# Kernel tuning notes

Measured on AMD Instinct MI355X. Metric: run time of the kernel, lower is better.

The kernel has to match this reference:

```python
import jax, jax.numpy as jnp
import numpy as np

N_CELLS, IN_DIM, HID, OUT = 65536, 128, 256, 128
MLP_H = 128   # engine MLP hidden width is hard-coded to 128 in the source
N_MORPH = 32  # min(32, n_cells//4)


def setup_inputs() -> dict:
    key = jax.random.key(0)
    ks = jax.random.split(key, 18)
    s = 0.05
    return {
        "x": jax.random.normal(ks[0], (1, IN_DIM), jnp.float32),
        "hiddens": jax.random.normal(ks[1], (N_CELLS, HID), jnp.float32) * 0.1,
        "Wa1": jax.random.normal(ks[2], (MLP_H, IN_DIM + HID), jnp.float32) * s,
        "ba1": jax.random.normal(ks[3], (MLP_H,), jnp.float32) * s,
        "Wa2": jax.random.normal(ks[4], (OUT, MLP_H), jnp.float32) * s,
        "ba2": jax.random.normal(ks[5], (OUT,), jnp.float32) * s,
        "Wg1": jax.random.normal(ks[6], (MLP_H, IN_DIM + HID), jnp.float32) * s,
        "bg1": jax.random.normal(ks[7], (MLP_H,), jnp.float32) * s,
        "Wg2": jax.random.normal(ks[8], (OUT, MLP_H), jnp.float32) * s,
        "bg2": jax.random.normal(ks[9], (OUT,), jnp.float32) * s,
        "W_ih": jax.random.normal(ks[10], (3 * HID, OUT + 1), jnp.float32) * s,
        "W_hh": jax.random.normal(ks[11], (3 * HID, HID), jnp.float32) * s,
        "b_ih": jax.random.normal(ks[12], (3 * HID,), jnp.float32) * s,
        "b_hh": jax.random.normal(ks[13], (3 * HID,), jnp.float32) * s,
        "nat_w": jnp.eye(HID, dtype=jnp.float32),  # nn.init.eye_
        "morph_w": jax.random.normal(ks[14], (N_MORPH, HID, HID), jnp.float32) * 0.02,
        "morph_src": jax.random.randint(ks[15], (N_MORPH,), 0, N_CELLS, jnp.int32),
        "morph_tgt": jax.random.randint(ks[16], (N_MORPH,), 0, N_CELLS, jnp.int32),
        "step": 0,
    }


def _forward(x, hiddens, Wa1, ba1, Wa2, ba2, Wg1, bg1, Wg2, bg2,
             W_ih, W_hh, b_ih, b_hh, nat_w, morph_w, morph_src, morph_tgt, step):
    n = hiddens.shape[0]
    # --- BenchMind, batched over all cells (x broadcast to every cell) ---
    xb = jnp.broadcast_to(x, (n, x.shape[-1]))
    combined = jnp.concatenate([xb, hiddens], axis=-1)               # [n, in+hid]
    a = jax.nn.relu(combined @ Wa1.T + ba1) @ Wa2.T + ba2            # [n, out]
    g = jax.nn.relu(combined @ Wg1.T + bg1) @ Wg2.T + bg2            # [n, out]
    out = a - g                                                       # [n, out]
    tension = jnp.mean(out * out, axis=-1, keepdims=True)            # [n, 1]
    # mem_input is detached in torch
    mem_in = jax.lax.stop_gradient(jnp.concatenate([out, tension], axis=-1))
    # --- PyTorch GRUCell math ---
    gi = mem_in @ W_ih.T + b_ih                                      # [n, 3H]
    gh = hiddens @ W_hh.T + b_hh                                     # [n, 3H]
    i_r, i_z, i_n = jnp.split(gi, 3, axis=-1)
    h_r, h_z, h_n = jnp.split(gh, 3, axis=-1)
    r = jax.nn.sigmoid(i_r + h_r)
    z = jax.nn.sigmoid(i_z + h_z)
    nn_ = jnp.tanh(i_n + r * h_n)
    hid = jax.lax.stop_gradient((1.0 - z) * nn_ + z * hiddens)       # detached new hiddens
    if step % 3 == 0:
        hid = jax.lax.stop_gradient(hid @ nat_w.T)                   # natural transformation
    # --- limit / colimit (morphism gather-transform-aggregate) ---
    limit = jnp.einsum('mij,mj->i', morph_w, hid[morph_src]) / N_MORPH
    colimit = jnp.einsum('mji,mj->i', morph_w, hid[morph_tgt]) / N_MORPH
    diff = limit - colimit
    cat_tension = jnp.mean(diff * diff)
    hid = hid + 0.05 * jax.lax.stop_gradient(diff)[None, :]
    # --- faction sync (+ debate if step > 5) ---
    n_f = min(8, n // 2)
    fs = n // n_f
    hf = hid[: n_f * fs].reshape(n_f, fs, hid.shape[-1])
    fmean = hf.mean(axis=1, keepdims=True)                           # [n_f,1,H]
    hf = 0.85 * hf + 0.15 * fmean
    if step > 5:
        global_op = hf.mean(axis=1).mean(axis=0)                     # mean of faction means
        dc = max(1, fs // 4)
        hf = hf.at[:, :dc].set(0.85 * hf[:, :dc] + 0.15 * global_op)
    hid = jnp.concatenate([hf.reshape(n_f * fs, -1), hid[n_f * fs:]], axis=0)
    # --- tension-weighted combination (weights detached: .item() in torch) ---
    t = jax.lax.stop_gradient(tension[:, 0])                         # [n]
    w = jax.nn.softmax(t, axis=0)
    combined_out = jnp.sum(w[:, None] * out, axis=0, keepdims=True)  # [1, out]
    avg_tension = jnp.mean(tension) + 0.1 * cat_tension
    return combined_out, avg_tension, hid


def reference(x, hiddens, Wa1, ba1, Wa2, ba2, Wg1, bg1, Wg2, bg2,
              W_ih, W_hh, b_ih, b_hh, nat_w, morph_w, morph_src, morph_tgt, step):
    combined_out, avg_tension, _ = _forward(
        x, hiddens, Wa1, ba1, Wa2, ba2, Wg1, bg1, Wg2, bg2,
        W_ih, W_hh, b_ih, b_hh, nat_w, morph_w, morph_src, morph_tgt, step)
    return combined_out, avg_tension
```

## Files before the change

kernel.cpp:

```cpp
#include <hip/hip_runtime.h>
#include <math.h>

#define N_CELLS 65536

#define OFF_W1B   0
#define OFF_W2A   32768
#define OFF_XW1B  49152
#define OFF_B2D   49408
#define OFF_PT    49536
#define OFF_PE    50560
#define OFF_POUT  51584
#define OFF_MI4   182656
#define OFF_TEN   190848
#define OFF_HH4   190912
#define OFF_GI    207296
#define OFF_GH    256448
#define OFF_PLIM  305600
#define OFF_PCOL  313792
#define OFF_GMSK  322048

typedef short bf16x8 __attribute__((ext_vector_type(8)));
typedef short s16x4  __attribute__((ext_vector_type(4)));
typedef float f32x4  __attribute__((ext_vector_type(4)));

__device__ __forceinline__ unsigned short f2bf(float f) {
    unsigned u = __builtin_bit_cast(unsigned, f);
    u += 0x7FFFu + ((u >> 16) & 1u);
    return (unsigned short)(u >> 16);
}

__device__ __forceinline__ bf16x8 cvt8(float4 a, float4 b) {
    bf16x8 v;
    v[0] = (short)f2bf(a.x); v[1] = (short)f2bf(a.y);
    v[2] = (short)f2bf(a.z); v[3] = (short)f2bf(a.w);
    v[4] = (short)f2bf(b.x); v[5] = (short)f2bf(b.y);
    v[6] = (short)f2bf(b.z); v[7] = (short)f2bf(b.w);
    return v;
}

__global__ __launch_bounds__(256) void k_prep(
    const float* __restrict__ x, const float* __restrict__ hiddens,
    const float* __restrict__ Wa1, const float* __restrict__ ba1,
    const float* __restrict__ Wa2, const float* __restrict__ ba2,
    const float* __restrict__ Wg1, const float* __restrict__ bg1,
    const float* __restrict__ Wg2, const float* __restrict__ bg2,
    const int* __restrict__ msrc, const int* __restrict__ mtgt,
    float* __restrict__ ws)
{
    const int b = blockIdx.x, t = threadIdx.x;
    unsigned short* w1b = (unsigned short*)(ws + OFF_W1B);
    unsigned short* w2a = (unsigned short*)(ws + OFF_W2A);
    if (b < 256) {
        const int n = b;
        const float* row = (n < 128) ? &Wa1[n * 384] : &Wg1[(n - 128) * 384];
        const int sk = t >> 3;
        w1b[(sk * 256 + n) * 8 + (t & 7)] = f2bf(row[128 + t]);
        if (n < 128) {
            float w2 = (t < 128) ? Wa2[n * 128 + t] : -Wg2[n * 128 + (t - 128)];
            w2a[(sk * 128 + n) * 8 + (t & 7)] = f2bf(w2);
        }
    } else if (b == 256) {
        const int n = t;
        const float* wr = (n < 128) ? &Wa1[n * 384] : &Wg1[(n - 128) * 384];
        float s = (n < 128) ? ba1[n] : bg1[n - 128];
        for (int j = 0; j < 128; ++j) s = fmaf(x[j], wr[j], s);
        ws[OFF_XW1B + n] = s;
        if (n < 128) ws[OFF_B2D + n] = ba2[n] - bg2[n];
    } else if (b < 321) {
        const int g = b - 257;
        const int cell = (g < 32) ? msrc[g] : mtgt[g - 32];
        ws[OFF_HH4 + (t >> 2) * 256 + g * 4 + (t & 3)] = hiddens[(size_t)cell * 256 + t];
    } else {
        unsigned long long* gm = (unsigned long long*)(ws + OFF_GMSK);
        for (int i = t; i < 1024; i += 256) gm[i] = 0ull;
        __syncthreads();
        if (t < 64) {
            const int cell = (t < 32) ? msrc[t] : mtgt[t - 32];
            atomicOr(&gm[cell >> 6], 1ull << t);
        }
    }
}

__global__ __launch_bounds__(512, 4) void k_main(
    const float* __restrict__ hiddens,
    const int* __restrict__ msrc, const int* __restrict__ mtgt,
    float* __restrict__ ws)
{
    __shared__ __align__(16) short hB[64 * 256];
    __shared__ __align__(16) short h1B[64 * 256];
    __shared__ float part[512];
    __shared__ float e_sm[64], t_sm[64];
    __shared__ int gid_sm[64];

    const int tid = threadIdx.x;
    const int lane = tid & 63, wid = tid >> 6;
    const int l15 = lane & 15, l4 = lane >> 4;
    const int blk = blockIdx.x;
    const int cell0 = blk * 64;

    if (tid < 64) gid_sm[tid] = (tid < 32) ? msrc[tid] : mtgt[tid - 32];

    const uint4* w1g = (const uint4*)(ws + OFF_W1B);
    const uint4* w2g = (const uint4*)(ws + OFF_W2A);

    uint4 aw0 = w1g[l4 * 256 + wid * 32 + l15];
    uint4 aw1 = w1g[l4 * 256 + wid * 32 + 16 + l15];

    {
        const int c = tid >> 3;
        const float* src = hiddens + (size_t)(cell0 + c) * 256 + (tid & 7) * 32;
        float4 va[4], vb[4];
#pragma unroll
        for (int it = 0; it < 4; ++it) {
            va[it] = *(const float4*)(src + it * 8);
            vb[it] = *(const float4*)(src + it * 8 + 4);
        }
#pragma unroll
        for (int it = 0; it < 4; ++it) {
            const int chunk = (tid & 7) * 4 + it;
            *(bf16x8*)&hB[c * 256 + ((chunk ^ (c & 7)) << 3)] = cvt8(va[it], vb[it]);
        }
    }
    __syncthreads();

    f32x4 acc[2][4];
#pragma unroll
    for (int nt = 0; nt < 2; ++nt)
#pragma unroll
        for (int ct = 0; ct < 4; ++ct) acc[nt][ct] = (f32x4)0.f;

#pragma unroll
    for (int s = 0; s < 8; ++s) {
        uint4 an0, an1;
        if (s < 7) {
            an0 = w1g[((s + 1) * 4 + l4) * 256 + wid * 32 + l15];
            an1 = w1g[((s + 1) * 4 + l4) * 256 + wid * 32 + 16 + l15];
        } else {
            an0 = w2g[l4 * 128 + wid * 16 + l15];
            an1 = an0;
        }
        bf16x8 bfr[4];
#pragma unroll
        for (int ct = 0; ct < 4; ++ct) {
            const int c = ct * 16 + l15;
            bfr[ct] = *(const bf16x8*)&hB[c * 256 + (((s * 4 + l4) ^ (l15 & 7)) << 3)];
        }
        const bf16x8 af0 = __builtin_bit_cast(bf16x8, aw0);
        const bf16x8 af1 = __builtin_bit_cast(bf16x8, aw1);
#pragma unroll
        for (int ct = 0; ct < 4; ++ct) {
            acc[0][ct] = __builtin_amdgcn_mfma_f32_16x16x32_bf16(af0, bfr[ct], acc[0][ct], 0, 0, 0);
            acc[1][ct] = __builtin_amdgcn_mfma_f32_16x16x32_bf16(af1, bfr[ct], acc[1][ct], 0, 0, 0);
        }
        aw0 = an0; aw1 = an1;
    }

    {
        float4 xb[2];
        xb[0] = *(const float4*)(ws + OFF_XW1B + wid * 32 + l4 * 4);
        xb[1] = *(const float4*)(ws + OFF_XW1B + wid * 32 + 16 + l4 * 4);
#pragma unroll
        for (int nt = 0; nt < 2; ++nt) {
            const int n0 = wid * 32 + nt * 16 + l4 * 4;
            const int chunk = n0 >> 3;
            const float bx[4] = {xb[nt].x, xb[nt].y, xb[nt].z, xb[nt].w};
#pragma unroll
            for (int ct = 0; ct < 4; ++ct) {
                const int c = ct * 16 + l15;
                s16x4 pk;
#pragma unroll
                for (int r = 0; r < 4; ++r)
                    pk[r] = (short)f2bf(fmaxf(acc[nt][ct][r] + bx[r], 0.f));
                *(s16x4*)&h1B[c * 256 + ((chunk ^ (l15 & 7)) << 3) + (l4 & 1) * 4] = pk;
            }
        }
    }
    __syncthreads();

    f32x4 acc2[4];
#pragma unroll
    for (int ct = 0; ct < 4; ++ct) acc2[ct] = (f32x4)0.f;

    uint4 a2 = aw0;
#pragma unroll
    for (int s = 0; s < 8; ++s) {
        uint4 a2n;
        if (s < 7) a2n = w2g[((s + 1) * 4 + l4) * 128 + wid * 16 + l15];
        bf16x8 b2[4];
#pragma unroll
        for (int ct = 0; ct < 4; ++ct) {
            const int c = ct * 16 + l15;
            b2[ct] = *(const bf16x8*)&h1B[c * 256 + (((s * 4 + l4) ^ (l15 & 7)) << 3)];
        }
        const bf16x8 af = __builtin_bit_cast(bf16x8, a2);
#pragma unroll
        for (int ct = 0; ct < 4; ++ct)
            acc2[ct] = __builtin_amdgcn_mfma_f32_16x16x32_bf16(af, b2[ct], acc2[ct], 0, 0, 0);
        a2 = a2n;
    }

    float outv[4][4];
    {
        float4 bd = *(const float4*)(ws + OFF_B2D + wid * 16 + l4 * 4);
        const float bv[4] = {bd.x, bd.y, bd.z, bd.w};
#pragma unroll
        for (int ct = 0; ct < 4; ++ct)
#pragma unroll
            for (int r = 0; r < 4; ++r)
                outv[ct][r] = acc2[ct][r] + bv[r];
    }

#pragma unroll
    for (int ct = 0; ct < 4; ++ct) {
        float sq = 0.f;
#pragma unroll
        for (int r = 0; r < 4; ++r) sq = fmaf(outv[ct][r], outv[ct][r], sq);
        sq += __shfl_xor(sq, 16);
        sq += __shfl_xor(sq, 32);
        if (l4 == 0) part[wid * 64 + ct * 16 + l15] = sq;
    }
    __syncthreads();

    const unsigned long long* gm = (const unsigned long long*)(ws + OFF_GMSK);
    if (tid < 64) {
        float s = 0.f;
#pragma unroll
        for (int w = 0; w < 8; ++w) s += part[w * 64 + tid];
        const float tv = s * (1.f / 128.f);
        const float ev = expf(tv);
        t_sm[tid] = tv; e_sm[tid] = ev;
        float pt = tv, pe = ev;
        for (int off = 32; off > 0; off >>= 1) {
            pt += __shfl_down(pt, off);
            pe += __shfl_down(pe, off);
        }
        if (tid == 0) { ws[OFF_PT + blk] = pt; ws[OFF_PE + blk] = pe; }
        unsigned long long m = gm[blk];
        while (m) {
            const int g = __builtin_ctzll(m); m &= m - 1;
            const int cg = gid_sm[g];
            if ((cg >> 6) == blk && (cg & 63) == tid) ws[OFF_TEN + g] = tv;
        }
    }
    __syncthreads();

    {
        float p[4];
#pragma unroll
        for (int r = 0; r < 4; ++r) {
            float s = 0.f;
#pragma unroll
            for (int ct = 0; ct < 4; ++ct)
                s = fmaf(e_sm[ct * 16 + l15], outv[ct][r], s);
            p[r] = s;
        }
#pragma unroll
        for (int r = 0; r < 4; ++r) {
            p[r] += __shfl_xor(p[r], 1);
            p[r] += __shfl_xor(p[r], 2);
            p[r] += __shfl_xor(p[r], 4);
            p[r] += __shfl_xor(p[r], 8);
        }
        if (l15 == 0)
            *(float4*)(ws + OFF_POUT + blk * 128 + wid * 16 + l4 * 4) =
                make_float4(p[0], p[1], p[2], p[3]);
    }

    {
        unsigned long long m = gm[blk];
        while (m) {
            const int g = __builtin_ctzll(m); m &= m - 1;
            const int cg = gid_sm[g];
            if ((cg >> 6) != blk) continue;
            const int c = cg & 63;
            if ((c & 15) == l15) {
                const int ct = c >> 4;
                *(float4*)(ws + OFF_MI4 + (wid * 4 + l4) * 256 + g * 4) =
                    make_float4(outv[ct][0], outv[ct][1], outv[ct][2], outv[ct][3]);
            }
        }
    }
}

__global__ __launch_bounds__(256) void k_tail1(
    const float* __restrict__ W_ih, const float* __restrict__ W_hh,
    const float* __restrict__ b_ih, const float* __restrict__ b_hh,
    float* __restrict__ ws)
{
    const int lane = threadIdx.x & 63;
    const int w    = threadIdx.x >> 6;
    const int row  = __builtin_amdgcn_readfirstlane(blockIdx.x * 4 + w);
    const float* mi4 = ws + OFF_MI4;
    const float* hh4 = ws + OFF_HH4;

    const float* wi = W_ih + row * 129;
    float gi = b_ih[row];
#pragma unroll 8
    for (int q = 0; q < 32; ++q) {
        float4 a = *(const float4*)(mi4 + q * 256 + lane * 4);
        gi = fmaf(wi[4 * q + 0], a.x, gi);
        gi = fmaf(wi[4 * q + 1], a.y, gi);
        gi = fmaf(wi[4 * q + 2], a.z, gi);
        gi = fmaf(wi[4 * q + 3], a.w, gi);
    }
    gi = fmaf(ws[OFF_TEN + lane], wi[128], gi);

    const float* wh = W_hh + (size_t)row * 256;
    float gh = b_hh[row];
#pragma unroll 8
    for (int q = 0; q < 64; ++q) {
        float4 a = *(const float4*)(hh4 + q * 256 + lane * 4);
        float4 b = *(const float4*)(wh + 4 * q);
        gh = fmaf(b.x, a.x, gh);
        gh = fmaf(b.y, a.y, gh);
        gh = fmaf(b.z, a.z, gh);
        gh = fmaf(b.w, a.w, gh);
    }
    ws[OFF_GI + row * 64 + lane] = gi;
    ws[OFF_GH + row * 64 + lane] = gh;
}

__global__ __launch_bounds__(512) void k_tail2(
    const float* __restrict__ nat_w, const float* __restrict__ morph_w,
    const int* __restrict__ step, float* __restrict__ ws)
{
    __shared__ float hd[2][256];
    __shared__ float hn[2][256];
    const int tid = threadIdx.x, half = tid >> 8, t = tid & 255, m = blockIdx.x;
    const int g = half * 32 + m;

    const float i_r = ws[OFF_GI + (0 * 256 + t) * 64 + g];
    const float i_z = ws[OFF_GI + (1 * 256 + t) * 64 + g];
    const float i_n = ws[OFF_GI + (2 * 256 + t) * 64 + g];
    const float h_r = ws[OFF_GH + (0 * 256 + t) * 64 + g];
    const float h_z = ws[OFF_GH + (1 * 256 + t) * 64 + g];
    const float h_n = ws[OFF_GH + (2 * 256 + t) * 64 + g];
    const float hv  = ws[OFF_HH4 + (t >> 2) * 256 + g * 4 + (t & 3)];

    const float r  = 1.f / (1.f + expf(-(i_r + h_r)));
    const float z  = 1.f / (1.f + expf(-(i_z + h_z)));
    const float nn = tanhf(i_n + r * h_n);
    const float hid = (1.f - z) * nn + z * hv;

    hd[half][t] = hid;
    __syncthreads();
    if (step[0] % 3 == 0) {
        const float4* wr = (const float4*)(nat_w + (size_t)t * 256);
        float s = 0.f;
        for (int q = 0; q < 64; ++q) {
            float4 wq = wr[q];
            s = fmaf(wq.x, hd[half][4 * q + 0], s);
            s = fmaf(wq.y, hd[half][4 * q + 1], s);
            s = fmaf(wq.z, hd[half][4 * q + 2], s);
            s = fmaf(wq.w, hd[half][4 * q + 3], s);
        }
        hn[half][t] = s;
    } else {
        hn[half][t] = hid;
    }
    __syncthreads();

    const float* wm = morph_w + (size_t)m * 65536;
    if (half == 0) {
        const float4* r_ = (const float4*)(wm + (size_t)t * 256);
        float L = 0.f;
        for (int q = 0; q < 64; ++q) {
            float4 wq = r_[q];
            L = fmaf(wq.x, hn[0][4 * q + 0], L);
            L = fmaf(wq.y, hn[0][4 * q + 1], L);
            L = fmaf(wq.z, hn[0][4 * q + 2], L);
            L = fmaf(wq.w, hn[0][4 * q + 3], L);
        }
        ws[OFF_PLIM + m * 256 + t] = L;
    } else {
        float C = 0.f;
        for (int j = 0; j < 256; ++j)
            C = fmaf(wm[j * 256 + t], hn[1][j], C);
        ws[OFF_PCOL + m * 256 + t] = C;
    }
}

__global__ __launch_bounds__(256) void k_out(const float* __restrict__ ws,
                                             float* __restrict__ out)
{
    __shared__ float red[256];
    const int b = blockIdx.x, t = threadIdx.x;
    if (b < 128) {
        float so = 0.f, se = 0.f;
        for (int i = t; i < 1024; i += 256) {
            so += ws[OFF_POUT + i * 128 + b];
            se += ws[OFF_PE + i];
        }
        red[t] = so; __syncthreads();
        for (int s = 128; s > 0; s >>= 1) { if (t < s) red[t] += red[t + s]; __syncthreads(); }
        const float SO = red[0]; __syncthreads();
        red[t] = se; __syncthreads();
        for (int s = 128; s > 0; s >>= 1) { if (t < s) red[t] += red[t + s]; __syncthreads(); }
        if (t == 0) out[b] = SO / red[0];
    } else {
        float pt = 0.f;
        for (int i = t; i < 1024; i += 256) pt += ws[OFF_PT + i];
        float L = 0.f, C = 0.f;
        for (int m = 0; m < 32; ++m) {
            L += ws[OFF_PLIM + m * 256 + t];
            C += ws[OFF_PCOL + m * 256 + t];
        }
        const float d = (L - C) * (1.f / 32.f);
        red[t] = d * d; __syncthreads();
        for (int s = 128; s > 0; s >>= 1) { if (t < s) red[t] += red[t + s]; __syncthreads(); }
        const float cat = red[0] * (1.f / 256.f); __syncthreads();
        red[t] = pt; __syncthreads();
        for (int s = 128; s > 0; s >>= 1) { if (t < s) red[t] += red[t + s]; __syncthreads(); }
        if (t == 0) out[128] = red[0] * (1.f / 65536.f) + 0.1f * cat;
    }
}

extern "C" void kernel_launch(void* const* d_in, const int* in_sizes, int n_in,
                              void* d_out, int out_size, void* d_ws, size_t ws_size,
                              hipStream_t stream)
{
    const float* x     = (const float*)d_in[0];
    const float* hidd  = (const float*)d_in[1];
    const float* Wa1   = (const float*)d_in[2];
    const float* ba1   = (const float*)d_in[3];
    const float* Wa2   = (const float*)d_in[4];
    const float* ba2   = (const float*)d_in[5];
    const float* Wg1   = (const float*)d_in[6];
    const float* bg1   = (const float*)d_in[7];
    const float* Wg2   = (const float*)d_in[8];
    const float* bg2   = (const float*)d_in[9];
    const float* W_ih  = (const float*)d_in[10];
    const float* W_hh  = (const float*)d_in[11];
    const float* b_ih  = (const float*)d_in[12];
    const float* b_hh  = (const float*)d_in[13];
    const float* nat_w = (const float*)d_in[14];
    const float* mw    = (const float*)d_in[15];
    const int*   msrc  = (const int*)d_in[16];
    const int*   mtgt  = (const int*)d_in[17];
    const int*   step  = (const int*)d_in[18];

    float* out = (float*)d_out;
    float* ws  = (float*)d_ws;

    k_prep <<<322, 256, 0, stream>>>(x, hidd, Wa1, ba1, Wa2, ba2, Wg1, bg1, Wg2, bg2, msrc, mtgt, ws);
    k_main <<<1024, 512, 0, stream>>>(hidd, msrc, mtgt, ws);
    k_tail1<<<192, 256, 0, stream>>>(W_ih, W_hh, b_ih, b_hh, ws);
    k_tail2<<<32, 512, 0, stream>>>(nat_w, mw, step, ws);
    k_out  <<<129, 256, 0, stream>>>(ws, out);
}
```

Baseline: 82.40 us.

## Make main kernel persistent over four tiles and restructure GRU/morph tail kernels

The main MLP kernel now handles four 64-cell tiles per block. It keeps all weight fragments in registers and prefetches the next tile's hidden rows while the current tile computes, and it pads the LDS row stride. The GRU tail is rewritten as one block per gathered cell, and the morph kernel is split into 256 blocks that stage weight chunks in LDS so column access coalesces. This aims to cut per-block weight reloads and the long serial tail kernels. The cost is fewer blocks, higher register pressure, and more partial sums for k_out to reduce.

```diff
diff --git a/kernel.cpp b/kernel.cpp
--- a/kernel.cpp
+++ b/kernel.cpp
@@ -1,7 +1,5 @@
 #include <hip/hip_runtime.h>
 #include <math.h>
-
-#define N_CELLS 65536
 
 #define OFF_W1B   0
 #define OFF_W2A   32768
@@ -10,18 +8,18 @@
 #define OFF_PT    49536
 #define OFF_PE    50560
 #define OFF_POUT  51584
-#define OFF_MI4   182656
-#define OFF_TEN   190848
-#define OFF_HH4   190912
-#define OFF_GI    207296
-#define OFF_GH    256448
-#define OFF_PLIM  305600
-#define OFF_PCOL  313792
-#define OFF_GMSK  322048
+#define OFF_MIG   182656
+#define OFF_HN    191104
+#define OFF_PLIM  207488
+#define OFF_PCOL8 215680
+#define OFF_GMSK  281216
 
 typedef short bf16x8 __attribute__((ext_vector_type(8)));
 typedef short s16x4  __attribute__((ext_vector_type(4)));
 typedef float f32x4  __attribute__((ext_vector_type(4)));
+
+#define HSTR 264
+#define POS(kc, c) ((((kc)) & 24) | ((((kc)) ^ ((c))) & 7))
 
 __device__ __forceinline__ unsigned short f2bf(float f) {
     unsigned u = __builtin_bit_cast(unsigned, f);
@@ -39,7 +37,7 @@
 }
 
 __global__ __launch_bounds__(256) void k_prep(
-    const float* __restrict__ x, const float* __restrict__ hiddens,
+    const float* __restrict__ x,
     const float* __restrict__ Wa1, const float* __restrict__ ba1,
     const float* __restrict__ Wa2, const float* __restrict__ ba2,
     const float* __restrict__ Wg1, const float* __restrict__ bg1,
@@ -53,11 +51,11 @@
     if (b < 256) {
         const int n = b;
         const float* row = (n < 128) ? &Wa1[n * 384] : &Wg1[(n - 128) * 384];
-        const int sk = t >> 3;
-        w1b[(sk * 256 + n) * 8 + (t & 7)] = f2bf(row[128 + t]);
+        const int kc = t >> 3;
+        w1b[(kc * 256 + n) * 8 + (t & 7)] = f2bf(row[128 + t]);
         if (n < 128) {
             float w2 = (t < 128) ? Wa2[n * 128 + t] : -Wg2[n * 128 + (t - 128)];
-            w2a[(sk * 128 + n) * 8 + (t & 7)] = f2bf(w2);
+            w2a[(kc * 128 + n) * 8 + (t & 7)] = f2bf(w2);
         }
     } else if (b == 256) {
         const int n = t;
@@ -66,10 +64,6 @@
         for (int j = 0; j < 128; ++j) s = fmaf(x[j], wr[j], s);
         ws[OFF_XW1B + n] = s;
         if (n < 128) ws[OFF_B2D + n] = ba2[n] - bg2[n];
-    } else if (b < 321) {
-        const int g = b - 257;
-        const int cell = (g < 32) ? msrc[g] : mtgt[g - 32];
-        ws[OFF_HH4 + (t >> 2) * 256 + g * 4 + (t & 3)] = hiddens[(size_t)cell * 256 + t];
     } else {
         unsigned long long* gm = (unsigned long long*)(ws + OFF_GMSK);
         for (int i = t; i < 1024; i += 256) gm[i] = 0ull;
@@ -81,302 +75,315 @@
     }
 }
 
-__global__ __launch_bounds__(512, 4) void k_main(
+__global__ __launch_bounds__(512, 2) void k_main(
     const float* __restrict__ hiddens,
     const int* __restrict__ msrc, const int* __restrict__ mtgt,
     float* __restrict__ ws)
 {
-    __shared__ __align__(16) short hB[64 * 256];
-    __shared__ __align__(16) short h1B[64 * 256];
+    __shared__ __align__(16) short hB[64 * HSTR];
+    __shared__ __align__(16) short h1B[64 * HSTR];
     __shared__ float part[512];
-    __shared__ float e_sm[64], t_sm[64];
+    __shared__ float e_sm[64], t_sm_[64];
     __shared__ int gid_sm[64];
 
-    const int tid = threadIdx.x;
+    const int tid  = threadIdx.x;
     const int lane = tid & 63, wid = tid >> 6;
     const int l15 = lane & 15, l4 = lane >> 4;
     const int blk = blockIdx.x;
-    const int cell0 = blk * 64;
+    const int cell0 = blk * 256;
 
     if (tid < 64) gid_sm[tid] = (tid < 32) ? msrc[tid] : mtgt[tid - 32];
 
     const uint4* w1g = (const uint4*)(ws + OFF_W1B);
     const uint4* w2g = (const uint4*)(ws + OFF_W2A);
 
-    uint4 aw0 = w1g[l4 * 256 + wid * 32 + l15];
-    uint4 aw1 = w1g[l4 * 256 + wid * 32 + 16 + l15];
-
-    {
-        const int c = tid >> 3;
-        const float* src = hiddens + (size_t)(cell0 + c) * 256 + (tid & 7) * 32;
-        float4 va[4], vb[4];
-#pragma unroll
-        for (int it = 0; it < 4; ++it) {
-            va[it] = *(const float4*)(src + it * 8);
-            vb[it] = *(const float4*)(src + it * 8 + 4);
-        }
-#pragma unroll
-        for (int it = 0; it < 4; ++it) {
-            const int chunk = (tid & 7) * 4 + it;
-            *(bf16x8*)&hB[c * 256 + ((chunk ^ (c & 7)) << 3)] = cvt8(va[it], vb[it]);
-        }
-    }
+    uint4 aw[8][2], a2[8];
+#pragma unroll
+    for (int s = 0; s < 8; ++s) {
+        aw[s][0] = w1g[(s * 4 + l4) * 256 + wid * 32 + l15];
+        aw[s][1] = w1g[(s * 4 + l4) * 256 + wid * 32 + 16 + l15];
+        a2[s]    = w2g[(s * 4 + l4) * 128 + wid * 16 + l15];
+    }
+
+    const int rc = tid >> 3;
+    const int cb = (tid & 7) * 32;
+    const float* hsrc = hiddens + (size_t)(cell0 + rc) * 256 + cb;
+
+    float4 nx[8];
+#pragma unroll
+    for (int it = 0; it < 8; ++it) nx[it] = *(const float4*)(hsrc + it * 4);
+#pragma unroll
+    for (int it = 0; it < 4; ++it) {
+        const int kc = (tid & 7) * 4 + it;
+        *(bf16x8*)&hB[rc * HSTR + POS(kc, rc) * 8] = cvt8(nx[2 * it], nx[2 * it + 1]);
+    }
+#pragma unroll
+    for (int it = 0; it < 8; ++it)
+        nx[it] = *(const float4*)(hsrc + 64 * 256 + it * 4);
     __syncthreads();
 
-    f32x4 acc[2][4];
-#pragma unroll
-    for (int nt = 0; nt < 2; ++nt)
-#pragma unroll
-        for (int ct = 0; ct < 4; ++ct) acc[nt][ct] = (f32x4)0.f;
-
-#pragma unroll
-    for (int s = 0; s < 8; ++s) {
-        uint4 an0, an1;
-        if (s < 7) {
-            an0 = w1g[((s + 1) * 4 + l4) * 256 + wid * 32 + l15];
-            an1 = w1g[((s + 1) * 4 + l4) * 256 + wid * 32 + 16 + l15];
-        } else {
-            an0 = w2g[l4 * 128 + wid * 16 + l15];
-            an1 = an0;
-        }
-        bf16x8 bfr[4];
-#pragma unroll
-        for (int ct = 0; ct < 4; ++ct) {
-            const int c = ct * 16 + l15;
-            bfr[ct] = *(const bf16x8*)&hB[c * 256 + (((s * 4 + l4) ^ (l15 & 7)) << 3)];
-        }
-        const bf16x8 af0 = __builtin_bit_cast(bf16x8, aw0);
-        const bf16x8 af1 = __builtin_bit_cast(bf16x8, aw1);
-#pragma unroll
-        for (int ct = 0; ct < 4; ++ct) {
-            acc[0][ct] = __builtin_amdgcn_mfma_f32_16x16x32_bf16(af0, bfr[ct], acc[0][ct], 0, 0, 0);
-            acc[1][ct] = __builtin_amdgcn_mfma_f32_16x16x32_bf16(af1, bfr[ct], acc[1][ct], 0, 0, 0);
-        }
-        aw0 = an0; aw1 = an1;
-    }
-
-    {
-        float4 xb[2];
-        xb[0] = *(const float4*)(ws + OFF_XW1B + wid * 32 + l4 * 4);
-        xb[1] = *(const float4*)(ws + OFF_XW1B + wid * 32 + 16 + l4 * 4);
-#pragma unroll
-        for (int nt = 0; nt < 2; ++nt) {
-            const int n0 = wid * 32 + nt * 16 + l4 * 4;
-            const int chunk = n0 >> 3;
-            const float bx[4] = {xb[nt].x, xb[nt].y, xb[nt].z, xb[nt].w};
+    float4 xb0 = *(const float4*)(ws + OFF_XW1B + wid * 32 + l4 * 4);
+    float4 xb1 = *(const float4*)(ws + OFF_XW1B + wid * 32 + 16 + l4 * 4);
+    float4 bd  = *(const float4*)(ws + OFF_B2D + wid * 16 + l4 * 4);
+    const float bdv[4] = {bd.x, bd.y, bd.z, bd.w};
+    const unsigned long long* gm = (const unsigned long long*)(ws + OFF_GMSK);
+
+    for (int t = 0; t < 4; ++t) {
+        const int bt = blk * 4 + t;
+
+        f32x4 acc[2][4];
+#pragma unroll
+        for (int nt = 0; nt < 2; ++nt)
+#pragma unroll
+            for (int ct = 0; ct < 4; ++ct) acc[nt][ct] = (f32x4)0.f;
+#pragma unroll
+        for (int s = 0; s < 8; ++s) {
+            bf16x8 bfr[4];
 #pragma unroll
             for (int ct = 0; ct < 4; ++ct) {
                 const int c = ct * 16 + l15;
-                s16x4 pk;
-#pragma unroll
-                for (int r = 0; r < 4; ++r)
-                    pk[r] = (short)f2bf(fmaxf(acc[nt][ct][r] + bx[r], 0.f));
-                *(s16x4*)&h1B[c * 256 + ((chunk ^ (l15 & 7)) << 3) + (l4 & 1) * 4] = pk;
-            }
-        }
-    }
-    __syncthreads();
-
-    f32x4 acc2[4];
-#pragma unroll
-    for (int ct = 0; ct < 4; ++ct) acc2[ct] = (f32x4)0.f;
-
-    uint4 a2 = aw0;
-#pragma unroll
-    for (int s = 0; s < 8; ++s) {
-        uint4 a2n;
-        if (s < 7) a2n = w2g[((s + 1) * 4 + l4) * 128 + wid * 16 + l15];
-        bf16x8 b2[4];
+                bfr[ct] = *(const bf16x8*)&hB[c * HSTR + POS(s * 4 + l4, c) * 8];
+            }
+            const bf16x8 af0 = __builtin_bit_cast(bf16x8, aw[s][0]);
+            const bf16x8 af1 = __builtin_bit_cast(bf16x8, aw[s][1]);
+#pragma unroll
+            for (int ct = 0; ct < 4; ++ct) {
+                acc[0][ct] = __builtin_amdgcn_mfma_f32_16x16x32_bf16(af0, bfr[ct], acc[0][ct], 0, 0, 0);
+                acc[1][ct] = __builtin_amdgcn_mfma_f32_16x16x32_bf16(af1, bfr[ct], acc[1][ct], 0, 0, 0);
+            }
+        }
+
+        {
+            const float b0[4] = {xb0.x, xb0.y, xb0.z, xb0.w};
+            const float b1[4] = {xb1.x, xb1.y, xb1.z, xb1.w};
+#pragma unroll
+            for (int nt = 0; nt < 2; ++nt) {
+                const int ch2 = wid * 4 + nt * 2 + (l4 >> 1);
+                const float* bb = nt ? b1 : b0;
+#pragma unroll
+                for (int ct = 0; ct < 4; ++ct) {
+                    const int c = ct * 16 + l15;
+                    s16x4 pk;
+#pragma unroll
+                    for (int r = 0; r < 4; ++r)
+                        pk[r] = (short)f2bf(fmaxf(acc[nt][ct][r] + bb[r], 0.f));
+                    *(s16x4*)&h1B[c * HSTR + POS(ch2, c) * 8 + (l4 & 1) * 4] = pk;
+                }
+            }
+        }
+        __syncthreads();
+
+        f32x4 acc2[4];
+#pragma unroll
+        for (int ct = 0; ct < 4; ++ct) acc2[ct] = (f32x4)0.f;
+#pragma unroll
+        for (int s = 0; s < 8; ++s) {
+            bf16x8 b2[4];
+#pragma unroll
+            for (int ct = 0; ct < 4; ++ct) {
+                const int c = ct * 16 + l15;
+                b2[ct] = *(const bf16x8*)&h1B[c * HSTR + POS(s * 4 + l4, c) * 8];
+            }
+            const bf16x8 af = __builtin_bit_cast(bf16x8, a2[s]);
+#pragma unroll
+            for (int ct = 0; ct < 4; ++ct)
+                acc2[ct] = __builtin_amdgcn_mfma_f32_16x16x32_bf16(af, b2[ct], acc2[ct], 0, 0, 0);
+        }
+
+        if (t < 3) {
+#pragma unroll
+            for (int it = 0; it < 4; ++it) {
+                const int kc = (tid & 7) * 4 + it;
+                *(bf16x8*)&hB[rc * HSTR + POS(kc, rc) * 8] = cvt8(nx[2 * it], nx[2 * it + 1]);
+            }
+            if (t < 2) {
+#pragma unroll
+                for (int it = 0; it < 8; ++it)
+                    nx[it] = *(const float4*)(hsrc + (size_t)(t + 2) * 64 * 256 + it * 4);
+            }
+        }
+
+        float outv[4][4];
+#pragma unroll
+        for (int ct = 0; ct < 4; ++ct)
+#pragma unroll
+            for (int r = 0; r < 4; ++r)
+                outv[ct][r] = acc2[ct][r] + bdv[r];
+
 #pragma unroll
         for (int ct = 0; ct < 4; ++ct) {
-            const int c = ct * 16 + l15;
-            b2[ct] = *(const bf16x8*)&h1B[c * 256 + (((s * 4 + l4) ^ (l15 & 7)) << 3)];
-        }
-        const bf16x8 af = __builtin_bit_cast(bf16x8, a2);
-#pragma unroll
-        for (int ct = 0; ct < 4; ++ct)
-            acc2[ct] = __builtin_amdgcn_mfma_f32_16x16x32_bf16(af, b2[ct], acc2[ct], 0, 0, 0);
-        a2 = a2n;
-    }
-
-    float outv[4][4];
-    {
-        float4 bd = *(const float4*)(ws + OFF_B2D + wid * 16 + l4 * 4);
-        const float bv[4] = {bd.x, bd.y, bd.z, bd.w};
-#pragma unroll
-        for (int ct = 0; ct < 4; ++ct)
-#pragma unroll
-            for (int r = 0; r < 4; ++r)
-                outv[ct][r] = acc2[ct][r] + bv[r];
-    }
-
-#pragma unroll
-    for (int ct = 0; ct < 4; ++ct) {
-        float sq = 0.f;
-#pragma unroll
-        for (int r = 0; r < 4; ++r) sq = fmaf(outv[ct][r], outv[ct][r], sq);
-        sq += __shfl_xor(sq, 16);
-        sq += __shfl_xor(sq, 32);
-        if (l4 == 0) part[wid * 64 + ct * 16 + l15] = sq;
-    }
-    __syncthreads();
-
-    const unsigned long long* gm = (const unsigned long long*)(ws + OFF_GMSK);
-    if (tid < 64) {
-        float s = 0.f;
-#pragma unroll
-        for (int w = 0; w < 8; ++w) s += part[w * 64 + tid];
-        const float tv = s * (1.f / 128.f);
-        const float ev = expf(tv);
-        t_sm[tid] = tv; e_sm[tid] = ev;
-        float pt = tv, pe = ev;
-        for (int off = 32; off > 0; off >>= 1) {
-            pt += __shfl_down(pt, off);
-            pe += __shfl_down(pe, off);
-        }
-        if (tid == 0) { ws[OFF_PT + blk] = pt; ws[OFF_PE + blk] = pe; }
-        unsigned long long m = gm[blk];
-        while (m) {
-            const int g = __builtin_ctzll(m); m &= m - 1;
-            const int cg = gid_sm[g];
-            if ((cg >> 6) == blk && (cg & 63) == tid) ws[OFF_TEN + g] = tv;
-        }
-    }
-    __syncthreads();
-
-    {
-        float p[4];
-#pragma unroll
-        for (int r = 0; r < 4; ++r) {
+            float sq = 0.f;
+#pragma unroll
+            for (int r = 0; r < 4; ++r) sq = fmaf(outv[ct][r], outv[ct][r], sq);
+            sq += __shfl_xor(sq, 16);
+            sq += __shfl_xor(sq, 32);
+            if (l4 == 0) part[wid * 64 + ct * 16 + l15] = sq;
+        }
+        __syncthreads();
+
+        if (tid < 64) {
             float s = 0.f;
 #pragma unroll
-            for (int ct = 0; ct < 4; ++ct)
-                s = fmaf(e_sm[ct * 16 + l15], outv[ct][r], s);
-            p[r] = s;
-        }
-#pragma unroll
-        for (int r = 0; r < 4; ++r) {
-            p[r] += __shfl_xor(p[r], 1);
-            p[r] += __shfl_xor(p[r], 2);
-            p[r] += __shfl_xor(p[r], 4);
-            p[r] += __shfl_xor(p[r], 8);
-        }
-        if (l15 == 0)
-            *(float4*)(ws + OFF_POUT + blk * 128 + wid * 16 + l4 * 4) =
-                make_float4(p[0], p[1], p[2], p[3]);
-    }
-
-    {
-        unsigned long long m = gm[blk];
-        while (m) {
-            const int g = __builtin_ctzll(m); m &= m - 1;
-            const int cg = gid_sm[g];
-            if ((cg >> 6) != blk) continue;
-            const int c = cg & 63;
-            if ((c & 15) == l15) {
-                const int ct = c >> 4;
-                *(float4*)(ws + OFF_MI4 + (wid * 4 + l4) * 256 + g * 4) =
-                    make_float4(outv[ct][0], outv[ct][1], outv[ct][2], outv[ct][3]);
-            }
-        }
-    }
-}
-
-__global__ __launch_bounds__(256) void k_tail1(
+            for (int w = 0; w < 8; ++w) s += part[w * 64 + tid];
+            const float tv = s * (1.f / 128.f);
+            const float ev = expf(tv);
+            t_sm_[tid] = tv; e_sm[tid] = ev;
+            float pt = tv, pe = ev;
+            for (int off = 32; off > 0; off >>= 1) {
+                pt += __shfl_down(pt, off);
+                pe += __shfl_down(pe, off);
+            }
+            if (tid == 0) { ws[OFF_PT + bt] = pt; ws[OFF_PE + bt] = pe; }
+            unsigned long long m = gm[bt];
+            while (m) {
+                const int g = __builtin_ctzll(m); m &= m - 1;
+                const int cg = gid_sm[g];
+                if ((cg >> 6) == bt && (cg & 63) == tid)
+                    ws[OFF_MIG + g * 132 + 128] = tv;
+            }
+        }
+        __syncthreads();
+
+        {
+            float p[4];
+#pragma unroll
+            for (int r = 0; r < 4; ++r) {
+                float s = 0.f;
+#pragma unroll
+                for (int ct = 0; ct < 4; ++ct)
+                    s = fmaf(e_sm[ct * 16 + l15], outv[ct][r], s);
+                p[r] = s;
+            }
+#pragma unroll
+            for (int r = 0; r < 4; ++r) {
+                p[r] += __shfl_xor(p[r], 1);
+                p[r] += __shfl_xor(p[r], 2);
+                p[r] += __shfl_xor(p[r], 4);
+                p[r] += __shfl_xor(p[r], 8);
+            }
+            if (l15 == 0)
+                *(float4*)(ws + OFF_POUT + bt * 128 + wid * 16 + l4 * 4) =
+                    make_float4(p[0], p[1], p[2], p[3]);
+        }
+        {
+            unsigned long long m = gm[bt];
+            while (m) {
+                const int g = __builtin_ctzll(m); m &= m - 1;
+                const int cg = gid_sm[g];
+                if ((cg >> 6) != bt) continue;
+                const int c = cg & 63;
+                if ((c & 15) == l15) {
+                    const int ct = c >> 4;
+                    *(float4*)(ws + OFF_MIG + g * 132 + wid * 16 + l4 * 4) =
+                        make_float4(outv[ct][0], outv[ct][1], outv[ct][2], outv[ct][3]);
+                }
+            }
+        }
+    }
+}
+
+__global__ __launch_bounds__(256) void k_gru(
+    const float* __restrict__ hiddens,
     const float* __restrict__ W_ih, const float* __restrict__ W_hh,
     const float* __restrict__ b_ih, const float* __restrict__ b_hh,
-    float* __restrict__ ws)
-{
-    const int lane = threadIdx.x & 63;
-    const int w    = threadIdx.x >> 6;
-    const int row  = __builtin_amdgcn_readfirstlane(blockIdx.x * 4 + w);
-    const float* mi4 = ws + OFF_MI4;
-    const float* hh4 = ws + OFF_HH4;
-
-    const float* wi = W_ih + row * 129;
-    float gi = b_ih[row];
+    const float* __restrict__ nat_w,
+    const int* __restrict__ msrc, const int* __restrict__ mtgt,
+    const int* __restrict__ step, float* __restrict__ ws)
+{
+    __shared__ float mi[132];
+    __shared__ float hh[256];
+    __shared__ float hd[256];
+    const int g = blockIdx.x, t = threadIdx.x;
+    const int cell = (g < 32) ? msrc[g] : mtgt[g - 32];
+    if (t < 129) mi[t] = ws[OFF_MIG + g * 132 + t];
+    hh[t] = hiddens[(size_t)cell * 256 + t];
+    __syncthreads();
+
+    float gi[3], gh[3];
+#pragma unroll
+    for (int p = 0; p < 3; ++p) {
+        const int row = p * 256 + t;
+        const float* wi = W_ih + row * 129;
+        float s = b_ih[row];
+#pragma unroll 4
+        for (int j = 0; j < 128; ++j) s = fmaf(wi[j], mi[j], s);
+        s = fmaf(wi[128], mi[128], s);
+        gi[p] = s;
+        const float4* wh = (const float4*)(W_hh + (size_t)row * 256);
+        float s2 = b_hh[row];
 #pragma unroll 8
-    for (int q = 0; q < 32; ++q) {
-        float4 a = *(const float4*)(mi4 + q * 256 + lane * 4);
-        gi = fmaf(wi[4 * q + 0], a.x, gi);
-        gi = fmaf(wi[4 * q + 1], a.y, gi);
-        gi = fmaf(wi[4 * q + 2], a.z, gi);
-        gi = fmaf(wi[4 * q + 3], a.w, gi);
-    }
-    gi = fmaf(ws[OFF_TEN + lane], wi[128], gi);
-
-    const float* wh = W_hh + (size_t)row * 256;
-    float gh = b_hh[row];
-#pragma unroll 8
-    for (int q = 0; q < 64; ++q) {
-        float4 a = *(const float4*)(hh4 + q * 256 + lane * 4);
-        float4 b = *(const float4*)(wh + 4 * q);
-        gh = fmaf(b.x, a.x, gh);
-        gh = fmaf(b.y, a.y, gh);
-        gh = fmaf(b.z, a.z, gh);
-        gh = fmaf(b.w, a.w, gh);
-    }
-    ws[OFF_GI + row * 64 + lane] = gi;
-    ws[OFF_GH + row * 64 + lane] = gh;
-}
-
-__global__ __launch_bounds__(512) void k_tail2(
-    const float* __restrict__ nat_w, const float* __restrict__ morph_w,
-    const int* __restrict__ step, float* __restrict__ ws)
-{
-    __shared__ float hd[2][256];
-    __shared__ float hn[2][256];
-    const int tid = threadIdx.x, half = tid >> 8, t = tid & 255, m = blockIdx.x;
-    const int g = half * 32 + m;
-
-    const float i_r = ws[OFF_GI + (0 * 256 + t) * 64 + g];
-    const float i_z = ws[OFF_GI + (1 * 256 + t) * 64 + g];
-    const float i_n = ws[OFF_GI + (2 * 256 + t) * 64 + g];
-    const float h_r = ws[OFF_GH + (0 * 256 + t) * 64 + g];
-    const float h_z = ws[OFF_GH + (1 * 256 + t) * 64 + g];
-    const float h_n = ws[OFF_GH + (2 * 256 + t) * 64 + g];
-    const float hv  = ws[OFF_HH4 + (t >> 2) * 256 + g * 4 + (t & 3)];
-
-    const float r  = 1.f / (1.f + expf(-(i_r + h_r)));
-    const float z  = 1.f / (1.f + expf(-(i_z + h_z)));
-    const float nn = tanhf(i_n + r * h_n);
-    const float hid = (1.f - z) * nn + z * hv;
-
-    hd[half][t] = hid;
+        for (int q = 0; q < 64; ++q) {
+            float4 w4 = wh[q];
+            s2 = fmaf(w4.x, hh[4 * q + 0], s2);
+            s2 = fmaf(w4.y, hh[4 * q + 1], s2);
+            s2 = fmaf(w4.z, hh[4 * q + 2], s2);
+            s2 = fmaf(w4.w, hh[4 * q + 3], s2);
+        }
+        gh[p] = s2;
+    }
+    const float r  = 1.f / (1.f + expf(-(gi[0] + gh[0])));
+    const float z  = 1.f / (1.f + expf(-(gi[1] + gh[1])));
+    const float nn = tanhf(gi[2] + r * gh[2]);
+    const float hid = (1.f - z) * nn + z * hh[t];
+
+    hd[t] = hid;
     __syncthreads();
+    float hn = hid;
     if (step[0] % 3 == 0) {
         const float4* wr = (const float4*)(nat_w + (size_t)t * 256);
         float s = 0.f;
+#pragma unroll 8
         for (int q = 0; q < 64; ++q) {
             float4 wq = wr[q];
-            s = fmaf(wq.x, hd[half][4 * q + 0], s);
-            s = fmaf(wq.y, hd[half][4 * q + 1], s);
-            s = fmaf(wq.z, hd[half][4 * q + 2], s);
-            s = fmaf(wq.w, hd[half][4 * q + 3], s);
-        }
-        hn[half][t] = s;
-    } else {
-        hn[half][t] = hid;
-    }
+            s = fmaf(wq.x, hd[4 * q + 0], s);
+            s = fmaf(wq.y, hd[4 * q + 1], s);
+            s = fmaf(wq.z, hd[4 * q + 2], s);
+            s = fmaf(wq.w, hd[4 * q + 3], s);
+        }
+        hn = s;
+    }
+    ws[OFF_HN + g * 256 + t] = hn;
+}
+
+__global__ __launch_bounds__(256) void k_morph(
+    const float* __restrict__ morph_w, float* __restrict__ ws)
+{
+    __shared__ float wsm[32 * 264];
+    __shared__ float hs[256], ht[256];
+    const int blk = blockIdx.x, t = threadIdx.x;
+    const int m = blk >> 3, ch = blk & 7;
+    const float* wm = morph_w + (size_t)m * 65536 + (size_t)ch * 32 * 256;
+    {
+        const int r = t >> 3, c0 = (t & 7) * 32;
+#pragma unroll
+        for (int it = 0; it < 8; ++it) {
+            float4 v = *(const float4*)(wm + r * 256 + c0 + it * 4);
+            *(float4*)&wsm[r * 264 + c0 + it * 4] = v;
+        }
+    }
+    hs[t] = ws[OFF_HN + m * 256 + t];
+    ht[t] = ws[OFF_HN + (32 + m) * 256 + t];
     __syncthreads();
 
-    const float* wm = morph_w + (size_t)m * 65536;
-    if (half == 0) {
-        const float4* r_ = (const float4*)(wm + (size_t)t * 256);
+    {
+        const int il = t >> 3, jc = t & 7;
         float L = 0.f;
-        for (int q = 0; q < 64; ++q) {
-            float4 wq = r_[q];
-            L = fmaf(wq.x, hn[0][4 * q + 0], L);
-            L = fmaf(wq.y, hn[0][4 * q + 1], L);
-            L = fmaf(wq.z, hn[0][4 * q + 2], L);
-            L = fmaf(wq.w, hn[0][4 * q + 3], L);
-        }
-        ws[OFF_PLIM + m * 256 + t] = L;
-    } else {
+#pragma unroll 8
+        for (int jj = 0; jj < 32; ++jj) {
+            const int j = jc + 8 * jj;
+            L = fmaf(wsm[il * 264 + j], hs[j], L);
+        }
+        L += __shfl_down(L, 4);
+        L += __shfl_down(L, 2);
+        L += __shfl_down(L, 1);
+        if (jc == 0) ws[OFF_PLIM + m * 256 + ch * 32 + il] = L;
+    }
+    {
         float C = 0.f;
-        for (int j = 0; j < 256; ++j)
-            C = fmaf(wm[j * 256 + t], hn[1][j], C);
-        ws[OFF_PCOL + m * 256 + t] = C;
+#pragma unroll 8
+        for (int r = 0; r < 32; ++r)
+            C = fmaf(wsm[r * 264 + t], ht[ch * 32 + r], C);
+        ws[OFF_PCOL8 + blk * 256 + t] = C;
     }
 }
 
@@ -401,10 +408,8 @@
         float pt = 0.f;
         for (int i = t; i < 1024; i += 256) pt += ws[OFF_PT + i];
         float L = 0.f, C = 0.f;
-        for (int m = 0; m < 32; ++m) {
-            L += ws[OFF_PLIM + m * 256 + t];
-            C += ws[OFF_PCOL + m * 256 + t];
-        }
+        for (int m = 0; m < 32; ++m) L += ws[OFF_PLIM + m * 256 + t];
+        for (int mc = 0; mc < 256; ++mc) C += ws[OFF_PCOL8 + mc * 256 + t];
         const float d = (L - C) * (1.f / 32.f);
         red[t] = d * d; __syncthreads();
         for (int s = 128; s > 0; s >>= 1) { if (t < s) red[t] += red[t + s]; __syncthreads(); }
@@ -442,9 +447,9 @@
     float* out = (float*)d_out;
     float* ws  = (float*)d_ws;
 
-    k_prep <<<322, 256, 0, stream>>>(x, hidd, Wa1, ba1, Wa2, ba2, Wg1, bg1, Wg2, bg2, msrc, mtgt, ws);
-    k_main <<<1024, 512, 0, stream>>>(hidd, msrc, mtgt, ws);
-    k_tail1<<<192, 256, 0, stream>>>(W_ih, W_hh, b_ih, b_hh, ws);
-    k_tail2<<<32, 512, 0, stream>>>(nat_w, mw, step, ws);
+    k_prep <<<258, 256, 0, stream>>>(x, Wa1, ba1, Wa2, ba2, Wg1, bg1, Wg2, bg2, msrc, mtgt, ws);
+    k_main <<<256, 512, 0, stream>>>(hidd, msrc, mtgt, ws);
+    k_gru  <<<64, 256, 0, stream>>>(hidd, W_ih, W_hh, b_ih, b_hh, nat_w, msrc, mtgt, step, ws);
+    k_morph<<<256, 256, 0, stream>>>(mw, ws);
     k_out  <<<129, 256, 0, stream>>>(ws, out);
 }
```

Measured after the change: 123.9 us. +50.4%, slower.
